# Kernel tuning notes

Measured on AMD Instinct MI355X. Metric: run time of the kernel, lower is better.

## Reference

```python
import jax, jax.numpy as jnp
import numpy as np

LAM = 100000.0  # lam default in ExemplarHead


def setup_inputs() -> dict:
    key = jax.random.key(0)
    T, n_way, n_shot, n_query, d = 32, 5, 5, 75, 1024
    k1, k2, k3 = jax.random.split(key, 3)
    query = jax.random.normal(k1, (T, n_query, d), dtype=jnp.float32)
    support = jax.random.normal(k2, (T, n_way * n_shot, d), dtype=jnp.float32)
    # original: np.random.normal(0, 4, (T*n_shot, d)) drawn per class -> (n_way, T, n_shot, d)
    noise = 4.0 * jax.random.normal(k3, (n_way, T, n_shot, d), dtype=jnp.float32)
    # labels sorted per task so the original nonzero-gather == reshape
    support_labels = jnp.tile(jnp.repeat(jnp.arange(n_way), n_shot), (T, 1))
    return {"query": query, "support": support, "noise": noise,
            "support_labels": support_labels, "n_way": n_way, "n_shot": n_shot}


def reference(query, support, noise, support_labels, n_way, n_shot):
    T, n_query, d = query.shape
    # per-class support gather (labels are [0..0,1..1,...] per task) + noise
    R = support.reshape(T, n_way, n_shot, d) + jnp.transpose(noise, (1, 0, 2, 3))
    Rt = jnp.swapaxes(R, 2, 3)                      # (T, n_way, d, n_shot)
    mean = Rt.mean(axis=3, keepdims=True)           # (T, n_way, d, 1)
    Rc = Rt - mean                                  # centered class reps
    Qc = query[:, None, :, :] - jnp.swapaxes(mean, 2, 3)  # (T, n_way, n_query, d)
    # batched reduced SVD of (d x n_shot) matrices
    u, s, _ = jnp.linalg.svd(Rc, full_matrices=False)     # u: (T, n_way, d, k)
    ss2 = (s ** 2) / (LAM + s ** 2)                        # (T, n_way, k)
    # proj = u @ diag(ss2) @ u^T @ Rc, then transpose -> (T, n_way, n_shot, d)
    A = jnp.einsum('twdk,twds->twks', u, Rc)
    proj = jnp.einsum('twdk,twk,twks->twsd', u, ss2, A)
    # squared euclidean distances: (T, n_way, n_query, n_shot)
    dist = jnp.sum((Qc[:, :, :, None, :] - proj[:, :, None, :, :]) ** 2, axis=-1)
    logits = -jnp.swapaxes(dist, 1, 2) / d          # (T, n_query, n_way, n_shot)
    return logits
```

## Files before the change

### kernel.cpp

```cpp
#include <hip/hip_runtime.h>


constexpr int   T_   = 32;
constexpr int   NW   = 5;
constexpr int   NS   = 5;
constexpr int   NQ   = 75;
constexpr int   D    = 1024;
constexpr int   D4   = D / 4;
constexpr float LAM  = 100000.0f;

__global__ __launch_bounds__(256) void exemplar_head_kernel(
    const float* __restrict__ query,
    const float* __restrict__ support,
    const float* __restrict__ noise,
    float* __restrict__ out)
{
    const int t    = blockIdx.x;
    const int w    = blockIdx.y;
    const int tid  = threadIdx.x;
    const int lane = tid & 63;
    const int wave = tid >> 6;

    __shared__ float Cs[NS][D];
    __shared__ float meanS[D];
    __shared__ float gpart[4][15];
    __shared__ float Ms[NS][NS];
    __shared__ float pdS[NS];

    const float4* sup4 = (const float4*)(support + (size_t)(t * NW * NS + w * NS) * D);
    const float4* noi4 = (const float4*)(noise   + (size_t)((w * T_ + t) * NS) * D);
    float4 r[NS];
    float4 sum = make_float4(0.f, 0.f, 0.f, 0.f);
#pragma unroll
    for (int s = 0; s < NS; ++s) {
        float4 a = sup4[s * D4 + tid];
        float4 b = noi4[s * D4 + tid];
        float4 v = make_float4(a.x + b.x, a.y + b.y, a.z + b.z, a.w + b.w);
        r[s] = v;
        sum.x += v.x; sum.y += v.y; sum.z += v.z; sum.w += v.w;
    }
    float4 mn = make_float4(sum.x * 0.2f, sum.y * 0.2f, sum.z * 0.2f, sum.w * 0.2f);
    ((float4*)meanS)[tid] = mn;
#pragma unroll
    for (int s = 0; s < NS; ++s) {
        r[s].x -= mn.x; r[s].y -= mn.y; r[s].z -= mn.z; r[s].w -= mn.w;
        ((float4*)Cs[s])[tid] = r[s];
    }

    float g[15];
    {
        int n = 0;
#pragma unroll
        for (int k = 0; k < NS; ++k)
#pragma unroll
            for (int l = k; l < NS; ++l) {
                g[n++] = r[k].x * r[l].x + r[k].y * r[l].y +
                         r[k].z * r[l].z + r[k].w * r[l].w;
            }
    }
#pragma unroll
    for (int off = 1; off < 64; off <<= 1)
#pragma unroll
        for (int n = 0; n < 15; ++n)
            g[n] += __shfl_xor(g[n], off, 64);
    if (lane == 0)
#pragma unroll
        for (int n = 0; n < 15; ++n) gpart[wave][n] = g[n];
    __syncthreads();

    if (tid == 0) {
        float G[NS][NS];
        int n = 0;
        for (int k = 0; k < NS; ++k)
            for (int l = k; l < NS; ++l) {
                float v = gpart[0][n] + gpart[1][n] + gpart[2][n] + gpart[3][n];
                ++n;
                G[k][l] = v; G[l][k] = v;
            }
        float A[NS][2 * NS];
        for (int i = 0; i < NS; ++i)
            for (int j = 0; j < NS; ++j) {
                A[i][j]      = G[i][j] + (i == j ? LAM : 0.0f);
                A[i][NS + j] = G[i][j];
            }
        for (int c = 0; c < NS; ++c) {
            float inv = 1.0f / A[c][c];
            for (int j = 0; j < 2 * NS; ++j) A[c][j] *= inv;
            for (int rI = 0; rI < NS; ++rI) {
                if (rI == c) continue;
                float f = A[rI][c];
                for (int j = 0; j < 2 * NS; ++j) A[rI][j] -= f * A[c][j];
            }
        }
        float M[NS][NS];
        for (int i = 0; i < NS; ++i)
            for (int j = 0; j < NS; ++j) {
                M[i][j] = A[i][NS + j];
                Ms[i][j] = M[i][j];
            }
        for (int s = 0; s < NS; ++s) {
            float acc = 0.f;
            for (int i = 0; i < NS; ++i) {
                float gi = 0.f;
                for (int j = 0; j < NS; ++j) gi += G[i][j] * M[j][s];
                acc += M[i][s] * gi;
            }
            pdS[s] = acc;
        }
    }
    __syncthreads();

    const float4* q4base = (const float4*)(query + (size_t)t * NQ * D);
    for (int q = wave; q < NQ; q += 4) {
        float v[NS] = {0.f, 0.f, 0.f, 0.f, 0.f};
        float sq = 0.f;
        const float4* q4 = q4base + q * D4;
#pragma unroll
        for (int j = 0; j < 4; ++j) {
            int i4 = lane + 64 * j;
            float4 qq = q4[i4];
            float4 m  = ((const float4*)meanS)[i4];
            float4 qc = make_float4(qq.x - m.x, qq.y - m.y, qq.z - m.z, qq.w - m.w);
            sq += qc.x * qc.x + qc.y * qc.y + qc.z * qc.z + qc.w * qc.w;
#pragma unroll
            for (int k = 0; k < NS; ++k) {
                float4 c = ((const float4*)Cs[k])[i4];
                v[k] += qc.x * c.x + qc.y * c.y + qc.z * c.z + qc.w * c.w;
            }
        }
#pragma unroll
        for (int off = 1; off < 64; off <<= 1) {
            sq += __shfl_xor(sq, off, 64);
#pragma unroll
            for (int k = 0; k < NS; ++k) v[k] += __shfl_xor(v[k], off, 64);
        }
        if (lane < NS) {
            const int s = lane;
            float dot = 0.f;
#pragma unroll
            for (int k = 0; k < NS; ++k) dot += v[k] * Ms[k][s];
            float dist = sq - 2.0f * dot + pdS[s];
            out[(((size_t)t * NQ + q) * NW + w) * NS + s] = -dist * (1.0f / (float)D);
        }
    }
}

extern "C" void kernel_launch(void* const* d_in, const int* in_sizes, int n_in,
                              void* d_out, int out_size, void* d_ws, size_t ws_size,
                              hipStream_t stream) {
    const float* query   = (const float*)d_in[0];
    const float* support = (const float*)d_in[1];
    const float* noise   = (const float*)d_in[2];
    float* out = (float*)d_out;

    dim3 grid(T_, NW);
    dim3 block(256);
    exemplar_head_kernel<<<grid, block, 0, stream>>>(query, support, noise, out);
}
```

Before: 90.57 us.

## Split into prep kernel and query-tiled kernel to raise grid parallelism

Moves per-(task,way) centering, Gram matrix and inverse computation into a separate prep kernel that writes C, mean, M and pd to workspace. A second kernel launches one block per (task, way, group of 4 queries), so there are many more blocks than the 160 that each looped serially over 75 queries. The cost is an extra launch, and each query block reloads the 20 KB centered support slice from workspace, mostly served from cache. The copy loop runs 6 iterations, covering 1536 float4 when the slice has 1280, so it writes past the end of CsF into meanS. That region is then overwritten by the meanS load in the same thread, so the overrun looks harmless.

```diff
diff --git a/kernel.cpp b/kernel.cpp
--- a/kernel.cpp
+++ b/kernel.cpp
@@ -9,23 +9,24 @@
 constexpr int   D4   = D / 4;
 constexpr float LAM  = 100000.0f;
 
-__global__ __launch_bounds__(256) void exemplar_head_kernel(
-    const float* __restrict__ query,
+constexpr size_t WS_C    = 0;
+constexpr size_t WS_MEAN = WS_C    + (size_t)T_ * NW * NS * D;
+constexpr size_t WS_M    = WS_MEAN + (size_t)T_ * NW * D;
+constexpr size_t WS_PD   = WS_M    + (size_t)T_ * NW * 25;
+
+__global__ __launch_bounds__(256) void prep_kernel(
     const float* __restrict__ support,
     const float* __restrict__ noise,
-    float* __restrict__ out)
+    float* __restrict__ ws)
 {
     const int t    = blockIdx.x;
     const int w    = blockIdx.y;
+    const int tw   = t * NW + w;
     const int tid  = threadIdx.x;
     const int lane = tid & 63;
     const int wave = tid >> 6;
 
-    __shared__ float Cs[NS][D];
-    __shared__ float meanS[D];
     __shared__ float gpart[4][15];
-    __shared__ float Ms[NS][NS];
-    __shared__ float pdS[NS];
 
     const float4* sup4 = (const float4*)(support + (size_t)(t * NW * NS + w * NS) * D);
     const float4* noi4 = (const float4*)(noise   + (size_t)((w * T_ + t) * NS) * D);
@@ -40,11 +41,14 @@
         sum.x += v.x; sum.y += v.y; sum.z += v.z; sum.w += v.w;
     }
     float4 mn = make_float4(sum.x * 0.2f, sum.y * 0.2f, sum.z * 0.2f, sum.w * 0.2f);
-    ((float4*)meanS)[tid] = mn;
+
+    float4* c4 = (float4*)(ws + WS_C + (size_t)tw * NS * D);
+    float4* m4 = (float4*)(ws + WS_MEAN + (size_t)tw * D);
+    m4[tid] = mn;
 #pragma unroll
     for (int s = 0; s < NS; ++s) {
         r[s].x -= mn.x; r[s].y -= mn.y; r[s].z -= mn.z; r[s].w -= mn.w;
-        ((float4*)Cs[s])[tid] = r[s];
+        c4[s * D4 + tid] = r[s];
     }
 
     float g[15];
@@ -53,10 +57,9 @@
 #pragma unroll
         for (int k = 0; k < NS; ++k)
 #pragma unroll
-            for (int l = k; l < NS; ++l) {
+            for (int l = k; l < NS; ++l)
                 g[n++] = r[k].x * r[l].x + r[k].y * r[l].y +
                          r[k].z * r[l].z + r[k].w * r[l].w;
-            }
     }
 #pragma unroll
     for (int off = 1; off < 64; off <<= 1)
@@ -96,7 +99,7 @@
         for (int i = 0; i < NS; ++i)
             for (int j = 0; j < NS; ++j) {
                 M[i][j] = A[i][NS + j];
-                Ms[i][j] = M[i][j];
+                ws[WS_M + (size_t)tw * 25 + i * NS + j] = M[i][j];
             }
         for (int s = 0; s < NS; ++s) {
             float acc = 0.f;
@@ -105,43 +108,73 @@
                 for (int j = 0; j < NS; ++j) gi += G[i][j] * M[j][s];
                 acc += M[i][s] * gi;
             }
-            pdS[s] = acc;
+            ws[WS_PD + (size_t)tw * NS + s] = acc;
         }
+    }
+}
+
+__global__ __launch_bounds__(256) void query_kernel(
+    const float* __restrict__ query,
+    const float* __restrict__ ws,
+    float* __restrict__ out)
+{
+    const int t    = blockIdx.x;
+    const int w    = blockIdx.y;
+    const int qt   = blockIdx.z;
+    const int tw   = t * NW + w;
+    const int tid  = threadIdx.x;
+    const int lane = tid & 63;
+    const int wave = tid >> 6;
+
+    __shared__ float CsF[NS * D];
+    __shared__ float meanS[D];
+    __shared__ float MsS[25];
+    __shared__ float pdS[NS];
+
+    {
+        const float4* csrc = (const float4*)(ws + WS_C + (size_t)tw * NS * D);
+        float4* cdst = (float4*)CsF;
+#pragma unroll
+        for (int i = 0; i < 6; ++i)
+            cdst[tid + 256 * i] = csrc[tid + 256 * i];
+        ((float4*)meanS)[tid] = ((const float4*)(ws + WS_MEAN + (size_t)tw * D))[tid];
+        if (tid < 25) MsS[tid] = ws[WS_M + (size_t)tw * 25 + tid];
+        if (tid >= 32 && tid < 32 + NS) pdS[tid - 32] = ws[WS_PD + (size_t)tw * NS + (tid - 32)];
     }
     __syncthreads();
 
-    const float4* q4base = (const float4*)(query + (size_t)t * NQ * D);
-    for (int q = wave; q < NQ; q += 4) {
-        float v[NS] = {0.f, 0.f, 0.f, 0.f, 0.f};
-        float sq = 0.f;
-        const float4* q4 = q4base + q * D4;
+    const int q = qt * 4 + wave;
+    if (q >= NQ) return;
+
+    const float4* q4 = (const float4*)(query + ((size_t)t * NQ + q) * D);
+    float v[NS] = {0.f, 0.f, 0.f, 0.f, 0.f};
+    float sq = 0.f;
 #pragma unroll
-        for (int j = 0; j < 4; ++j) {
-            int i4 = lane + 64 * j;
-            float4 qq = q4[i4];
-            float4 m  = ((const float4*)meanS)[i4];
-            float4 qc = make_float4(qq.x - m.x, qq.y - m.y, qq.z - m.z, qq.w - m.w);
-            sq += qc.x * qc.x + qc.y * qc.y + qc.z * qc.z + qc.w * qc.w;
+    for (int j = 0; j < 4; ++j) {
+        int i4 = lane + 64 * j;
+        float4 qq = q4[i4];
+        float4 m  = ((const float4*)meanS)[i4];
+        float4 qc = make_float4(qq.x - m.x, qq.y - m.y, qq.z - m.z, qq.w - m.w);
+        sq += qc.x * qc.x + qc.y * qc.y + qc.z * qc.z + qc.w * qc.w;
 #pragma unroll
-            for (int k = 0; k < NS; ++k) {
-                float4 c = ((const float4*)Cs[k])[i4];
-                v[k] += qc.x * c.x + qc.y * c.y + qc.z * c.z + qc.w * c.w;
-            }
+        for (int k = 0; k < NS; ++k) {
+            float4 c = ((const float4*)CsF)[k * D4 + i4];
+            v[k] += qc.x * c.x + qc.y * c.y + qc.z * c.z + qc.w * c.w;
         }
+    }
 #pragma unroll
-        for (int off = 1; off < 64; off <<= 1) {
-            sq += __shfl_xor(sq, off, 64);
+    for (int off = 1; off < 64; off <<= 1) {
+        sq += __shfl_xor(sq, off, 64);
 #pragma unroll
-            for (int k = 0; k < NS; ++k) v[k] += __shfl_xor(v[k], off, 64);
-        }
-        if (lane < NS) {
-            const int s = lane;
-            float dot = 0.f;
+        for (int k = 0; k < NS; ++k) v[k] += __shfl_xor(v[k], off, 64);
+    }
+    if (lane < NS) {
+        const int s = lane;
+        float dot = 0.f;
 #pragma unroll
-            for (int k = 0; k < NS; ++k) dot += v[k] * Ms[k][s];
-            float dist = sq - 2.0f * dot + pdS[s];
-            out[(((size_t)t * NQ + q) * NW + w) * NS + s] = -dist * (1.0f / (float)D);
-        }
+        for (int k = 0; k < NS; ++k) dot += v[k] * MsS[k * NS + s];
+        float dist = sq - 2.0f * dot + pdS[s];
+        out[(((size_t)t * NQ + q) * NW + w) * NS + s] = -dist * (1.0f / (float)D);
     }
 }
 
@@ -152,8 +185,11 @@
     const float* support = (const float*)d_in[1];
     const float* noise   = (const float*)d_in[2];
     float* out = (float*)d_out;
+    float* ws  = (float*)d_ws;
 
-    dim3 grid(T_, NW);
-    dim3 block(256);
-    exemplar_head_kernel<<<grid, block, 0, stream>>>(query, support, noise, out);
+    dim3 gridA(T_, NW);
+    prep_kernel<<<gridA, 256, 0, stream>>>(support, noise, ws);
+
+    dim3 gridB(T_, NW, (NQ + 3) / 4);
+    query_kernel<<<gridB, 256, 0, stream>>>(query, ws, out);
 }
```

Result: faster. 84.37 us (-6.8%).

## Split query range across grid z and process four queries per wave

Applied to the files above, without the earlier changes.

Adds a third grid dimension so each block handles 16 queries instead of all 75, raising block count from 160 to 800 to fill more CUs. Each wave now computes four queries at once, reusing each shared-memory class-vector load across them and batching the cross-lane reductions. The cost is that every block recomputes the support centering, Gram matrix and small inverse, so support and noise reads and that setup work repeat five times per (task, way).

```diff
diff --git a/kernel.cpp b/kernel.cpp
--- a/kernel.cpp
+++ b/kernel.cpp
@@ -9,7 +9,7 @@
 constexpr int   D4   = D / 4;
 constexpr float LAM  = 100000.0f;
 
-__global__ __launch_bounds__(256) void exemplar_head_kernel(
+__global__ __launch_bounds__(256) void exemplar_fused_kernel(
     const float* __restrict__ query,
     const float* __restrict__ support,
     const float* __restrict__ noise,
@@ -21,10 +21,10 @@
     const int lane = tid & 63;
     const int wave = tid >> 6;
 
-    __shared__ float Cs[NS][D];
+    __shared__ float CsF[NS * D];
     __shared__ float meanS[D];
     __shared__ float gpart[4][15];
-    __shared__ float Ms[NS][NS];
+    __shared__ float MsS[25];
     __shared__ float pdS[NS];
 
     const float4* sup4 = (const float4*)(support + (size_t)(t * NW * NS + w * NS) * D);
@@ -44,28 +44,27 @@
 #pragma unroll
     for (int s = 0; s < NS; ++s) {
         r[s].x -= mn.x; r[s].y -= mn.y; r[s].z -= mn.z; r[s].w -= mn.w;
-        ((float4*)Cs[s])[tid] = r[s];
+        ((float4*)CsF)[s * D4 + tid] = r[s];
     }
 
-    float g[15];
     {
+        float g[15];
         int n = 0;
 #pragma unroll
         for (int k = 0; k < NS; ++k)
 #pragma unroll
-            for (int l = k; l < NS; ++l) {
+            for (int l = k; l < NS; ++l)
                 g[n++] = r[k].x * r[l].x + r[k].y * r[l].y +
                          r[k].z * r[l].z + r[k].w * r[l].w;
-            }
+#pragma unroll
+        for (int off = 1; off < 64; off <<= 1)
+#pragma unroll
+            for (int m = 0; m < 15; ++m)
+                g[m] += __shfl_xor(g[m], off, 64);
+        if (lane == 0)
+#pragma unroll
+            for (int m = 0; m < 15; ++m) gpart[wave][m] = g[m];
     }
-#pragma unroll
-    for (int off = 1; off < 64; off <<= 1)
-#pragma unroll
-        for (int n = 0; n < 15; ++n)
-            g[n] += __shfl_xor(g[n], off, 64);
-    if (lane == 0)
-#pragma unroll
-        for (int n = 0; n < 15; ++n) gpart[wave][n] = g[n];
     __syncthreads();
 
     if (tid == 0) {
@@ -96,7 +95,7 @@
         for (int i = 0; i < NS; ++i)
             for (int j = 0; j < NS; ++j) {
                 M[i][j] = A[i][NS + j];
-                Ms[i][j] = M[i][j];
+                MsS[i * NS + j] = M[i][j];
             }
         for (int s = 0; s < NS; ++s) {
             float acc = 0.f;
@@ -110,36 +109,70 @@
     }
     __syncthreads();
 
+    const int qbase = blockIdx.z * 16 + wave * 4;
     const float4* q4base = (const float4*)(query + (size_t)t * NQ * D);
-    for (int q = wave; q < NQ; q += 4) {
-        float v[NS] = {0.f, 0.f, 0.f, 0.f, 0.f};
-        float sq = 0.f;
-        const float4* q4 = q4base + q * D4;
+
+    const float4* qp[4];
+    bool valid[4];
 #pragma unroll
-        for (int j = 0; j < 4; ++j) {
-            int i4 = lane + 64 * j;
-            float4 qq = q4[i4];
-            float4 m  = ((const float4*)meanS)[i4];
-            float4 qc = make_float4(qq.x - m.x, qq.y - m.y, qq.z - m.z, qq.w - m.w);
-            sq += qc.x * qc.x + qc.y * qc.y + qc.z * qc.z + qc.w * qc.w;
+    for (int qi = 0; qi < 4; ++qi) {
+        int q = qbase + qi;
+        valid[qi] = (q < NQ);
+        qp[qi] = q4base + (size_t)(valid[qi] ? q : 0) * D4;
+    }
+
+    float acc[4][NS];
+    float sq[4];
 #pragma unroll
-            for (int k = 0; k < NS; ++k) {
-                float4 c = ((const float4*)Cs[k])[i4];
-                v[k] += qc.x * c.x + qc.y * c.y + qc.z * c.z + qc.w * c.w;
-            }
+    for (int qi = 0; qi < 4; ++qi) {
+        sq[qi] = 0.f;
+#pragma unroll
+        for (int k = 0; k < NS; ++k) acc[qi][k] = 0.f;
+    }
+
+#pragma unroll
+    for (int j = 0; j < 4; ++j) {
+        const int i4 = lane + 64 * j;
+        float4 m = ((const float4*)meanS)[i4];
+        float4 qc[4];
+#pragma unroll
+        for (int qi = 0; qi < 4; ++qi) {
+            float4 qq = qp[qi][i4];
+            qc[qi] = make_float4(qq.x - m.x, qq.y - m.y, qq.z - m.z, qq.w - m.w);
+            sq[qi] += qc[qi].x * qc[qi].x + qc[qi].y * qc[qi].y +
+                      qc[qi].z * qc[qi].z + qc[qi].w * qc[qi].w;
         }
 #pragma unroll
-        for (int off = 1; off < 64; off <<= 1) {
-            sq += __shfl_xor(sq, off, 64);
+        for (int k = 0; k < NS; ++k) {
+            float4 c = ((const float4*)CsF)[k * D4 + i4];
 #pragma unroll
-            for (int k = 0; k < NS; ++k) v[k] += __shfl_xor(v[k], off, 64);
+            for (int qi = 0; qi < 4; ++qi)
+                acc[qi][k] += qc[qi].x * c.x + qc[qi].y * c.y +
+                              qc[qi].z * c.z + qc[qi].w * c.w;
         }
-        if (lane < NS) {
-            const int s = lane;
+    }
+
+#pragma unroll
+    for (int off = 1; off < 64; off <<= 1) {
+#pragma unroll
+        for (int qi = 0; qi < 4; ++qi) {
+            sq[qi] += __shfl_xor(sq[qi], off, 64);
+#pragma unroll
+            for (int k = 0; k < NS; ++k)
+                acc[qi][k] += __shfl_xor(acc[qi][k], off, 64);
+        }
+    }
+
+    if (lane < NS) {
+        const int s = lane;
+#pragma unroll
+        for (int qi = 0; qi < 4; ++qi) {
+            if (!valid[qi]) continue;
+            const int q = qbase + qi;
             float dot = 0.f;
 #pragma unroll
-            for (int k = 0; k < NS; ++k) dot += v[k] * Ms[k][s];
-            float dist = sq - 2.0f * dot + pdS[s];
+            for (int k = 0; k < NS; ++k) dot += acc[qi][k] * MsS[k * NS + s];
+            float dist = sq[qi] - 2.0f * dot + pdS[s];
             out[(((size_t)t * NQ + q) * NW + w) * NS + s] = -dist * (1.0f / (float)D);
         }
     }
@@ -153,7 +186,6 @@
     const float* noise   = (const float*)d_in[2];
     float* out = (float*)d_out;
 
-    dim3 grid(T_, NW);
-    dim3 block(256);
-    exemplar_head_kernel<<<grid, block, 0, stream>>>(query, support, noise, out);
+    dim3 grid(T_, NW, (NQ + 15) / 16);
+    exemplar_fused_kernel<<<grid, 256, 0, stream>>>(query, support, noise, out);
 }
```

Measured after the change: 86.99 us. 4.0% less time.
